# Performance work log

Measured on AMD Instinct MI355X. Metric: run time of the kernel, lower is better.

## Reference

```python
import jax, jax.numpy as jnp
import numpy as np

NH = 12
D = 768
HD = D // NH
F = 3072
EPS = 1e-6
SCALE = 1.0 / np.sqrt(HD).astype(np.float32)


def _ln(x, g, b):
    m = x.mean(-1, keepdims=True)
    v = ((x - m) ** 2).mean(-1, keepdims=True)
    return (x - m) / jnp.sqrt(v + EPS) * g + b


def _heads(t):
    B, S, _ = t.shape
    return t.reshape(B, S, NH, HD).transpose(0, 2, 1, 3)  # [B,H,S,hd]


def _attn(q, k, v):
    # q,k,v: [B,H,S,hd]; dropout rate is 0 so omitted
    s = jnp.einsum('bhqd,bhkd->bhqk', q, k) * SCALE
    p = jax.nn.softmax(s, axis=-1)
    c = jnp.einsum('bhqk,bhkd->bhqd', p, v)
    B, H, S, _ = c.shape
    return c.transpose(0, 2, 1, 3).reshape(B, S, D)


def _mlp(x, W1, b1, W2, b2):
    h = jax.nn.gelu(x @ W1 + b1)  # dropout rate 0.1 -> identity (eval)
    return h @ W2 + b2


def setup_inputs() -> dict:
    key = jax.random.key(0)
    ks = jax.random.split(key, 16)
    B, S = 4, 1024
    rnd = lambda k, sh: (jax.random.normal(k, sh, jnp.float32) * 0.02)
    inp = {
        'x': jax.random.normal(ks[0], (B, S, D), jnp.float32),
        'y': jax.random.normal(ks[1], (B, S, D), jnp.float32),
        'ln1x_g': jnp.ones((D,)), 'ln1x_b': jnp.zeros((D,)),
        'ln1y_g': jnp.ones((D,)), 'ln1y_b': jnp.zeros((D,)),
        'Wq': rnd(ks[2], (D, D)), 'bq': jnp.zeros((D,)),
        'Wk': rnd(ks[3], (D, D)), 'bk': jnp.zeros((D,)),
        'Wv': rnd(ks[4], (D, D)), 'bv': jnp.zeros((D,)),
        'Wo': rnd(ks[5], (D, D)), 'bo': jnp.zeros((D,)),
        'Wqd': rnd(ks[6], (D, D)), 'bqd': jnp.zeros((D,)),
        'Wkd': rnd(ks[7], (D, D)), 'bkd': jnp.zeros((D,)),
        'Wvd': rnd(ks[8], (D, D)), 'bvd': jnp.zeros((D,)),
        'Wod': rnd(ks[9], (D, D)), 'bod': jnp.zeros((D,)),
        'w11': jnp.full((1,), 0.5), 'w12': jnp.full((1,), 0.5),
        'w21': jnp.full((1,), 0.5), 'w22': jnp.full((1,), 0.5),
        'ln2x_g': jnp.ones((D,)), 'ln2x_b': jnp.zeros((D,)),
        'ln2y_g': jnp.ones((D,)), 'ln2y_b': jnp.zeros((D,)),
        'W1': rnd(ks[10], (D, F)), 'b1': jnp.zeros((F,)),
        'W2': rnd(ks[11], (F, D)), 'b2': jnp.zeros((D,)),
        'W1d': rnd(ks[12], (D, F)), 'b1d': jnp.zeros((F,)),
        'W2d': rnd(ks[13], (F, D)), 'b2d': jnp.zeros((D,)),
    }
    return inp


def reference(x, y, ln1x_g, ln1x_b, ln1y_g, ln1y_b,
              Wq, bq, Wk, bk, Wv, bv, Wo, bo,
              Wqd, bqd, Wkd, bkd, Wvd, bvd, Wod, bod,
              w11, w12, w21, w22,
              ln2x_g, ln2x_b, ln2y_g, ln2y_b,
              W1, b1, W2, b2, W1d, b1d, W2d, b2d):
    hx, hy = x, y
    xn = _ln(x, ln1x_g, ln1x_b)
    yn = _ln(y, ln1y_g, ln1y_b)
    q = _heads(xn @ Wq + bq); k = _heads(xn @ Wk + bk); v = _heads(xn @ Wv + bv)
    qd = _heads(yn @ Wqd + bqd); kd = _heads(yn @ Wkd + bkd); vd = _heads(yn @ Wvd + bvd)
    a_sx = _attn(q, k, v) @ Wo + bo          # self-x
    a_sy = _attn(qd, kd, vd) @ Wod + bod     # self-y
    a_cx = _attn(q, kd, vd) @ Wo + bo        # cross x-query into y
    a_cy = _attn(qd, k, v) @ Wod + bod       # cross y-query into x
    ax = w11 * a_sx + w12 * a_cx
    ay = w21 * a_sy + w22 * a_cy
    x = ax + hx
    y = ay + hy
    hx, hy = x, y
    x = _mlp(_ln(x, ln2x_g, ln2x_b), W1, b1, W2, b2) + hx
    y = _mlp(_ln(y, ln2y_g, ln2y_b), W1d, b1d, W2d, b2d) + hy
    return (x, y)
```

## Files before the change

### kernel.cpp

```cpp
#include <hip/hip_runtime.h>

typedef unsigned short u16;
typedef unsigned short u16x8 __attribute__((ext_vector_type(8)));
typedef short s16x8 __attribute__((ext_vector_type(8)));
typedef float f32x4 __attribute__((ext_vector_type(4)));

#define EL ((size_t)3145728)
#define DDE ((size_t)589824)
#define DFE ((size_t)2359296)

#if __has_builtin(__builtin_amdgcn_exp2f)
#define EXP2(x) __builtin_amdgcn_exp2f(x)
#else
#define EXP2(x) __expf((x) * 0.6931471805599453f)
#endif

__device__ __forceinline__ float b2f(u16 u) {
    return __builtin_bit_cast(float, (unsigned)u << 16);
}
__device__ __forceinline__ u16 f2bf(float f) {
    unsigned x = __builtin_bit_cast(unsigned, f);
    return (u16)((x + 0x7fffu + ((x >> 16) & 1u)) >> 16);
}
__device__ __forceinline__ float gelu_f(float x) {
    float t = x + 0.044715f * x * x * x;
    return x * __builtin_amdgcn_rcpf(1.0f + EXP2(-2.302207417f * t));
}
__device__ __forceinline__ f32x4 mfma16(s16x8 a, s16x8 b, f32x4 c) {
    return __builtin_amdgcn_mfma_f32_16x16x32_bf16(a, b, c, 0, 0, 0);
}
__device__ __forceinline__ void gld16(const u16* g, u16* l) {
    __builtin_amdgcn_global_load_lds((const __attribute__((address_space(1))) void*)g,
                                     (__attribute__((address_space(3))) void*)l,
                                     16, 0, 0);
}
__device__ __forceinline__ void xcd_map(int NN, int& m, int& n, int& z, int& ks) {
    int p = blockIdx.x, T = gridDim.x;
    int ppx = T >> 3;
    int xcd = p & 7, l = p >> 3;
    int panel = l / NN;
    n = l - panel * NN;
    int gp = xcd * (ppx / NN) + panel;
    m = gp & 31;
    z = (gp >> 5) & 1;
    ks = gp >> 6;
}

__global__ __launch_bounds__(256) void transpose8_k(const float* p0, const float* p1,
                                                    const float* p2, const float* p3,
                                                    const float* p4, const float* p5,
                                                    const float* p6, const float* p7,
                                                    u16* __restrict__ dst0) {
    int z = blockIdx.z;
    const float* in = z == 0 ? p0 : z == 1 ? p1 : z == 2 ? p2 : z == 3 ? p3
                    : z == 4 ? p4 : z == 5 ? p5 : z == 6 ? p6 : p7;
    u16* out = dst0 + (size_t)z * DDE;
    const int K = 768, N = 768;
    __shared__ u16 tile[64][72];
    int k0 = blockIdx.y << 6, n0 = blockIdx.x << 6;
    int tid = threadIdx.x;
    int r = tid >> 2, c = (tid & 3) << 4;
    const float* ip = in + (size_t)(k0 + r) * N + n0 + c;
#pragma unroll
    for (int q = 0; q < 4; ++q) {
        f32x4 v = *(const f32x4*)(ip + 4 * q);
#pragma unroll
        for (int e = 0; e < 4; ++e) tile[r][c + 4 * q + e] = f2bf(v[e]);
    }
    __syncthreads();
    u16x8 o0, o1;
#pragma unroll
    for (int e = 0; e < 8; ++e) { o0[e] = tile[c + e][r]; o1[e] = tile[c + 8 + e][r]; }
    u16* op = out + (size_t)(n0 + r) * K + k0 + c;
    *(u16x8*)op = o0;
    *(u16x8*)(op + 8) = o1;
}

__global__ __launch_bounds__(256) void transpose2_k(const float* pa, const float* pb,
                                                    u16* __restrict__ dst0, size_t dsz,
                                                    int K, int N) {
    int z = blockIdx.z;
    const float* in = z ? pb : pa;
    u16* out = dst0 + (size_t)z * dsz;
    __shared__ u16 tile[64][72];
    int k0 = blockIdx.y << 6, n0 = blockIdx.x << 6;
    int tid = threadIdx.x;
    int r = tid >> 2, c = (tid & 3) << 4;
    const float* ip = in + (size_t)(k0 + r) * N + n0 + c;
#pragma unroll
    for (int q = 0; q < 4; ++q) {
        f32x4 v = *(const f32x4*)(ip + 4 * q);
#pragma unroll
        for (int e = 0; e < 4; ++e) tile[r][c + 4 * q + e] = f2bf(v[e]);
    }
    __syncthreads();
    u16x8 o0, o1;
#pragma unroll
    for (int e = 0; e < 8; ++e) { o0[e] = tile[c + e][r]; o1[e] = tile[c + 8 + e][r]; }
    u16* op = out + (size_t)(n0 + r) * K + k0 + c;
    *(u16x8*)op = o0;
    *(u16x8*)(op + 8) = o1;
}

__global__ __launch_bounds__(256) void vtrans_k(const u16* __restrict__ Vrow,
                                                u16* __restrict__ VT0) {
    int st = blockIdx.x, bh = blockIdx.y, z = blockIdx.z;
    const u16* src = Vrow + (size_t)z * EL + ((size_t)bh << 16) + (size_t)st * 64 * 64;
    u16* dst = VT0 + (size_t)z * 3 * EL + ((size_t)bh << 16) + st * 64;
    __shared__ u16 tile[64][72];
    int tid = threadIdx.x;
    int r = tid >> 2, c = (tid & 3) << 4;
    const u16* ip = src + (size_t)r * 64 + c;
    u16x8 a = *(const u16x8*)ip;
    u16x8 b = *(const u16x8*)(ip + 8);
#pragma unroll
    for (int e = 0; e < 8; ++e) { tile[r][c + e] = a[e]; tile[r][c + 8 + e] = b[e]; }
    __syncthreads();
    u16x8 o0, o1;
#pragma unroll
    for (int e = 0; e < 8; ++e) { o0[e] = tile[c + e][r]; o1[e] = tile[c + 8 + e][r]; }
    u16* op = dst + (size_t)r * 1024 + c;
    *(u16x8*)op = o0;
    *(u16x8*)(op + 8) = o1;
}

__global__ __launch_bounds__(256) void ln_k(const float* __restrict__ inX,
                                            const float* __restrict__ inY,
                                            const float* gX, const float* bX,
                                            const float* gY, const float* bY,
                                            u16* __restrict__ out0) {
    int z = blockIdx.y;
    const float* in = z ? inY : inX;
    const float* g = z ? gY : gX;
    const float* be = z ? bY : bX;
    u16* out = out0 + (size_t)z * EL;
    int row = blockIdx.x, tid = threadIdx.x;
    const float* p = in + (size_t)row * 768;
    float v0 = p[tid], v1 = p[tid + 256], v2 = p[tid + 512];
    float s = v0 + v1 + v2;
    float q = v0 * v0 + v1 * v1 + v2 * v2;
#pragma unroll
    for (int m = 1; m < 64; m <<= 1) { s += __shfl_xor(s, m); q += __shfl_xor(q, m); }
    __shared__ float red[8];
    int w = tid >> 6, lane = tid & 63;
    if (lane == 0) { red[w] = s; red[4 + w] = q; }
    __syncthreads();
    s = red[0] + red[1] + red[2] + red[3];
    q = red[4] + red[5] + red[6] + red[7];
    float mean = s * (1.0f / 768.0f);
    float var = q * (1.0f / 768.0f) - mean * mean;
    float rstd = rsqrtf(var + 1e-6f);
    u16* o = out + (size_t)row * 768;
    o[tid]       = f2bf((v0 - mean) * rstd * g[tid]       + be[tid]);
    o[tid + 256] = f2bf((v1 - mean) * rstd * g[tid + 256] + be[tid + 256]);
    o[tid + 512] = f2bf((v2 - mean) * rstd * g[tid + 512] + be[tid + 512]);
}

__global__ __launch_bounds__(256) void lnb_k(const u16* __restrict__ inX,
                                             const u16* __restrict__ inY,
                                             const float* gX, const float* bX,
                                             const float* gY, const float* bY,
                                             u16* __restrict__ out0) {
    int z = blockIdx.y;
    const u16* in = z ? inY : inX;
    const float* g = z ? gY : gX;
    const float* be = z ? bY : bX;
    u16* out = out0 + (size_t)z * EL;
    int row = blockIdx.x, tid = threadIdx.x;
    const u16* p = in + (size_t)row * 768;
    float v0 = b2f(p[tid]), v1 = b2f(p[tid + 256]), v2 = b2f(p[tid + 512]);
    float s = v0 + v1 + v2;
    float q = v0 * v0 + v1 * v1 + v2 * v2;
#pragma unroll
    for (int m = 1; m < 64; m <<= 1) { s += __shfl_xor(s, m); q += __shfl_xor(q, m); }
    __shared__ float red[8];
    int w = tid >> 6, lane = tid & 63;
    if (lane == 0) { red[w] = s; red[4 + w] = q; }
    __syncthreads();
    s = red[0] + red[1] + red[2] + red[3];
    q = red[4] + red[5] + red[6] + red[7];
    float mean = s * (1.0f / 768.0f);
    float var = q * (1.0f / 768.0f) - mean * mean;
    float rstd = rsqrtf(var + 1e-6f);
    u16* o = out + (size_t)row * 768;
    o[tid]       = f2bf((v0 - mean) * rstd * g[tid]       + be[tid]);
    o[tid + 256] = f2bf((v1 - mean) * rstd * g[tid + 256] + be[tid + 256]);
    o[tid + 512] = f2bf((v2 - mean) * rstd * g[tid + 512] + be[tid + 512]);
}

__global__ __launch_bounds__(256) void blend_k(u16* __restrict__ a0,
                                               const u16* __restrict__ b0,
                                               const float* w11, const float* w12,
                                               const float* w21, const float* w22,
                                               int n8) {
    int z = blockIdx.z;
    u16* a = a0 + (size_t)z * EL;
    const u16* b = b0 + (size_t)z * EL;
    float wa = z ? *w21 : *w11, wb = z ? *w22 : *w12;
    for (int i = blockIdx.x * blockDim.x + threadIdx.x; i < n8;
         i += gridDim.x * blockDim.x) {
        u16x8 va = ((const u16x8*)a)[i];
        u16x8 vb = ((const u16x8*)b)[i];
        u16x8 r;
#pragma unroll
        for (int e = 0; e < 8; ++e) r[e] = f2bf(wa * b2f(va[e]) + wb * b2f(vb[e]));
        ((u16x8*)a)[i] = r;
    }
}

__global__ __launch_bounds__(256) void combine_k(const float* __restrict__ parts,
                                                 int KS,
                                                 const u16* __restrict__ x1b,
                                                 const float* __restrict__ b2X,
                                                 const float* __restrict__ b2Y,
                                                 float* __restrict__ out, int n4tot) {
    int i = blockIdx.x * 256 + threadIdx.x;
    if (i >= n4tot) return;
    size_t e = (size_t)i * 4;
    f32x4 s = ((const f32x4*)parts)[i];
    for (int k = 1; k < KS; ++k)
        s += ((const f32x4*)(parts + (size_t)k * 2 * EL))[i];
    const float* bb = (e < EL) ? b2X : b2Y;
    int n = (int)(e % 768);
    ushort4 xv = ((const ushort4*)x1b)[i];
    f32x4 r;
    r[0] = s[0] + bb[n]     + b2f(xv.x);
    r[1] = s[1] + bb[n + 1] + b2f(xv.y);
    r[2] = s[2] + bb[n + 2] + b2f(xv.z);
    r[3] = s[3] + bb[n + 3] + b2f(xv.w);
    ((f32x4*)out)[i] = r;
}

#define EPI_GELU 3
#define EPI_WO 4
#define EPI_MLP2 5
#define EPI_PART 6

template <int EPI>
__global__ __launch_bounds__(256) void gemm_k(
    const u16* __restrict__ A0, size_t Asz,
    const u16* __restrict__ B0, size_t Bsz,
    const float* __restrict__ bias0, const float* __restrict__ bias1,
    const void* __restrict__ r0, const void* __restrict__ r1,
    const float* s1a, const float* s1b, const float* s2a, const float* s2b,
    void* __restrict__ C0, size_t Csz,
    int M, int N, int K, int NN, int KS) {
    int m_, n_, z, ks;
    xcd_map(NN, m_, n_, z, ks);
    const int Kloc = K / KS;
    const u16* A = A0 + z * Asz;
    const u16* BT = B0 + z * Bsz;
    const float* bias = z ? bias1 : bias0;
    const float* residf = (const float*)(z ? r1 : r0);
    const u16* residb = (const u16*)(z ? r1 : r0);
    u16* Cb = (u16*)C0 + z * Csz;
    float* Cf = (float*)C0 + ((size_t)ks * 2 + z) * Csz;
    __shared__ u16 lA[2][4096];
    __shared__ u16 lB[2][4096];
    int tid = threadIdx.x;
    int bm0 = m_ << 7, bn0 = n_ << 7;
    int lane = tid & 63, wid = tid >> 6;
    int fr = lane & 15, g = lane >> 4;
    int wm = wid >> 1, wn = wid & 1;
    const u16* srcA0 = A + (size_t)(bm0 + (tid & 127)) * K + ks * Kloc + ((tid >> 7) << 3);
    const u16* srcA1 = srcA0 + 16;
    const u16* srcB0 = BT + (size_t)(bn0 + (tid & 127)) * K + ks * Kloc + ((tid >> 7) << 3);
    const u16* srcB1 = srcB0 + 16;
    auto STAGE = [&](int buf, int k0) {
        gld16(srcA0 + k0, &lA[buf][0] + tid * 8);
        gld16(srcA1 + k0, &lA[buf][0] + 2048 + tid * 8);
        gld16(srcB0 + k0, &lB[buf][0] + tid * 8);
        gld16(srcB1 + k0, &lB[buf][0] + 2048 + tid * 8);
    };
    f32x4 acc[4][4] = {};
    STAGE(0, 0);
    __syncthreads();
    int cur = 0;
    for (int k0 = 0; k0 < Kloc; k0 += 32) {
        if (k0 + 32 < Kloc) STAGE(cur ^ 1, k0 + 32);
        s16x8 af[4], bf[4];
#pragma unroll
        for (int i = 0; i < 4; ++i)
            af[i] = *(const s16x8*)&lA[cur][(g * 128 + wm * 64 + i * 16 + fr) * 8];
#pragma unroll
        for (int j = 0; j < 4; ++j)
            bf[j] = *(const s16x8*)&lB[cur][(g * 128 + wn * 64 + j * 16 + fr) * 8];
#pragma unroll
        for (int i = 0; i < 4; ++i)
#pragma unroll
            for (int j = 0; j < 4; ++j)
                acc[i][j] = mfma16(af[i], bf[j], acc[i][j]);
        __syncthreads();
        cur ^= 1;
    }
    float bscale = 1.0f;
    if (EPI == EPI_WO) bscale = z ? (s2a[0] + s2b[0]) : (s1a[0] + s1b[0]);
#pragma unroll
    for (int j = 0; j < 4; ++j) {
        int n = bn0 + wn * 64 + j * 16 + fr;
        float bv = 0.0f;
        if (EPI != EPI_PART) bv = bias[n] * bscale;
#pragma unroll
        for (int i = 0; i < 4; ++i) {
#pragma unroll
            for (int r = 0; r < 4; ++r) {
                int m = bm0 + wm * 64 + i * 16 + (g << 2) + r;
                size_t idx = (size_t)m * N + n;
                float v = acc[i][j][r] + bv;
                if (EPI == EPI_GELU) {
                    Cb[idx] = f2bf(gelu_f(v));
                } else if (EPI == EPI_WO) {
                    Cb[idx] = f2bf(v + residf[idx]);
                } else if (EPI == EPI_MLP2) {
                    Cf[idx] = v + b2f(residb[idx]);
                } else {
                    Cf[idx] = v;
                }
            }
        }
    }
}

__global__ __launch_bounds__(256) void gemm_qkv_k(const u16* __restrict__ A0,
                                                  const u16* __restrict__ B0,
                                                  const float* bq, const float* bk,
                                                  const float* bv, const float* bqd,
                                                  const float* bkd, const float* bvd,
                                                  u16* __restrict__ Qd,
                                                  u16* __restrict__ Kd,
                                                  u16* __restrict__ Vd) {
    const int K = 768;
    int m_, n_, z, ks_;
    xcd_map(18, m_, n_, z, ks_);
    const u16* A = A0 + z * EL;
    const u16* BT = B0 + z * 3 * DDE;
    __shared__ u16 lA[2][4096];
    __shared__ u16 lB[2][4096];
    int tid = threadIdx.x;
    int bm0 = m_ << 7, bn0 = n_ << 7;
    int lane = tid & 63, wid = tid >> 6, wm = wid >> 1, wn = wid & 1;
    int fr = lane & 15, g = lane >> 4;
    const u16* srcA0 = A + (size_t)(bm0 + (tid & 127)) * K + ((tid >> 7) << 3);
    const u16* srcA1 = srcA0 + 16;
    const u16* srcB0 = BT + (size_t)(bn0 + (tid & 127)) * K + ((tid >> 7) << 3);
    const u16* srcB1 = srcB0 + 16;
    auto STAGE = [&](int buf, int k0) {
        gld16(srcA0 + k0, &lA[buf][0] + tid * 8);
        gld16(srcA1 + k0, &lA[buf][0] + 2048 + tid * 8);
        gld16(srcB0 + k0, &lB[buf][0] + tid * 8);
        gld16(srcB1 + k0, &lB[buf][0] + 2048 + tid * 8);
    };
    f32x4 acc[4][4] = {};
    STAGE(0, 0);
    __syncthreads();
    int cur = 0;
    for (int k0 = 0; k0 < K; k0 += 32) {
        if (k0 + 32 < K) STAGE(cur ^ 1, k0 + 32);
        s16x8 af[4], bf[4];
#pragma unroll
        for (int i = 0; i < 4; ++i)
            af[i] = *(const s16x8*)&lA[cur][(g * 128 + wm * 64 + i * 16 + fr) * 8];
#pragma unroll
        for (int j = 0; j < 4; ++j)
            bf[j] = *(const s16x8*)&lB[cur][(g * 128 + wn * 64 + j * 16 + fr) * 8];
#pragma unroll
        for (int i = 0; i < 4; ++i)
#pragma unroll
            for (int j = 0; j < 4; ++j)
                acc[i][j] = mfma16(af[i], bf[j], acc[i][j]);
        __syncthreads();
        cur ^= 1;
    }
    int seg = bn0 / 768;
    const float* bp = seg == 0 ? (z ? bqd : bq) : seg == 1 ? (z ? bkd : bk) : (z ? bvd : bv);
    u16* out;
    size_t zoff;
    if (seg == 0)      { out = Qd; zoff = (size_t)z * 3 * EL; }
    else if (seg == 1) { out = Kd; zoff = (size_t)z * 3 * EL; }
    else               { out = Vd; zoff = (size_t)z * EL; }
    int nbase = bn0 - seg * 768;
    const float qs = (seg == 0) ? 0.180336880f : 1.0f;
#pragma unroll
    for (int j = 0; j < 4; ++j) {
        int nn = nbase + wn * 64 + j * 16 + fr;
        float bvl = bp[nn];
        int hh = nn >> 6, hd = nn & 63;
#pragma unroll
        for (int i = 0; i < 4; ++i) {
#pragma unroll
            for (int r = 0; r < 4; ++r) {
                int m = bm0 + wm * 64 + i * 16 + (g << 2) + r;
                int bb = m >> 10, ss = m & 1023;
                size_t o = zoff + (((size_t)(bb * 12 + hh)) << 16) + ((size_t)ss << 6) + hd;
                out[o] = f2bf((acc[i][j][r] + bvl) * qs);
            }
        }
    }
}

__global__ __launch_bounds__(256) void attn_k(const u16* __restrict__ Qx,
                                              const u16* __restrict__ Kx,
                                              const u16* __restrict__ VTx,
                                              const u16* __restrict__ Qy,
                                              const u16* __restrict__ Ky,
                                              const u16* __restrict__ VTy,
                                              u16* __restrict__ csx,
                                              u16* __restrict__ ccx,
                                              u16* __restrict__ csy,
                                              u16* __restrict__ ccy) {
    int p = blockIdx.x;
    int lg = (p & 7) * 192 + (p >> 3);
    int sg = lg >> 4, wi = lg & 15;
    int qt = wi & 7, sub = wi >> 3;
    int pairi = sg / 48, bh = sg % 48;
    int cfg = pairi == 0 ? (sub ? 3 : 0) : (sub ? 2 : 1);
    const u16 *Qp, *Kp, *Vp;
    u16* Op;
    if (cfg == 0)      { Qp = Qx; Kp = Kx; Vp = VTx; Op = csx; }
    else if (cfg == 1) { Qp = Qy; Kp = Ky; Vp = VTy; Op = csy; }
    else if (cfg == 2) { Qp = Qx; Kp = Ky; Vp = VTy; Op = ccx; }
    else               { Qp = Qy; Kp = Kx; Vp = VTx; Op = ccy; }
    const u16* Qh = Qp + ((size_t)bh << 16);
    const u16* Kh = Kp + ((size_t)bh << 16);
    const u16* Vh = Vp + ((size_t)bh << 16);
    int b = bh / 12, h = bh % 12;
    int tid = threadIdx.x, lane = tid & 63, w = tid >> 6;
    int q0 = qt * 128 + w * 32;
    int fr = lane & 15, ko = (lane >> 4) << 3, g = lane >> 4;
    bool glo = lane < 32;
    int srcA = fr + ((lane & 16) << 1);
    int srcB = srcA + 16;

    __shared__ u16 kls[4096];
    __shared__ u16 vls[4096];

    s16x8 qf[2][2];
#pragma unroll
    for (int s = 0; s < 2; ++s) {
        const u16* qp = Qh + (size_t)(q0 + s * 16 + fr) * 64 + ko;
        qf[s][0] = *(const s16x8*)qp;
        qf[s][1] = *(const s16x8*)(qp + 32);
    }

    f32x4 acc[2][4] = {};
    float lsum[2] = {0.f, 0.f};
    f32x4 zz = {0.f, 0.f, 0.f, 0.f};

    int krow = tid >> 3, kpc = tid & 7;
    int kgc = kpc ^ (krow & 7);
    int vdr = tid >> 2, vpv = tid & 3;
    int cK0 = ((fr << 3) + (g ^ (fr & 7))) << 3;
    int cK1 = ((fr << 3) + ((g + 4) ^ (fr & 7))) << 3;
    int cK2 = (((fr + 16) << 3) + (g ^ (fr & 7))) << 3;
    int cK3 = (((fr + 16) << 3) + ((g + 4) ^ (fr & 7))) << 3;

    auto HALF = [&](int base) {
        s16x8 Kf0 = *(const s16x8*)&kls[base + cK0];
        s16x8 Kf1 = *(const s16x8*)&kls[base + cK1];
        s16x8 Kf2 = *(const s16x8*)&kls[base + cK2];
        s16x8 Kf3 = *(const s16x8*)&kls[base + cK3];
        s16x8 Vf[4];
#pragma unroll
        for (int t4 = 0; t4 < 4; ++t4)
            Vf[t4] = *(const s16x8*)&vls[base + ((t4 * 16 + fr) << 5) + (g << 3)];
        s16x8 pa[2];
#pragma unroll
        for (int s = 0; s < 2; ++s) {
            __builtin_amdgcn_s_setprio(1);
            f32x4 t0 = mfma16(Kf0, qf[s][0], zz);
            t0 = mfma16(Kf1, qf[s][1], t0);
            f32x4 t1 = mfma16(Kf2, qf[s][0], zz);
            t1 = mfma16(Kf3, qf[s][1], t1);
            __builtin_amdgcn_s_setprio(0);
            float p00 = EXP2(t0[0]), p01 = EXP2(t0[1]);
            float p02 = EXP2(t0[2]), p03 = EXP2(t0[3]);
            float p10 = EXP2(t1[0]), p11 = EXP2(t1[1]);
            float p12 = EXP2(t1[2]), p13 = EXP2(t1[3]);
            lsum[s] += (p00 + p01 + p02 + p03) + (p10 + p11 + p12 + p13);
            unsigned w0, w1, w2, w3;
            asm("v_cvt_pk_bf16_f32 %0, %1, %2" : "=v"(w0) : "v"(p00), "v"(p01));
            asm("v_cvt_pk_bf16_f32 %0, %1, %2" : "=v"(w1) : "v"(p02), "v"(p03));
            asm("v_cvt_pk_bf16_f32 %0, %1, %2" : "=v"(w2) : "v"(p10), "v"(p11));
            asm("v_cvt_pk_bf16_f32 %0, %1, %2" : "=v"(w3) : "v"(p12), "v"(p13));
            int e0 = __shfl((int)w0, srcA), e1 = __shfl((int)w1, srcA);
            int e2 = __shfl((int)w0, srcB), e3 = __shfl((int)w1, srcB);
            int f0 = __shfl((int)w2, srcA), f1 = __shfl((int)w3, srcA);
            int f2 = __shfl((int)w2, srcB), f3 = __shfl((int)w3, srcB);
            int4 wd;
            wd.x = glo ? e0 : f0;
            wd.y = glo ? e1 : f1;
            wd.z = glo ? e2 : f2;
            wd.w = glo ? e3 : f3;
            pa[s] = __builtin_bit_cast(s16x8, wd);
        }
        __builtin_amdgcn_s_setprio(1);
#pragma unroll
        for (int t4 = 0; t4 < 4; ++t4) {
            acc[0][t4] = mfma16(pa[0], Vf[t4], acc[0][t4]);
            acc[1][t4] = mfma16(pa[1], Vf[t4], acc[1][t4]);
        }
        __builtin_amdgcn_s_setprio(0);
    };

    for (int kb = 0; kb < 1024; kb += 64) {
        gld16(Kh + (size_t)(kb + krow) * 64 + kgc * 8, &kls[tid * 8]);
        gld16(Kh + (size_t)(kb + 32 + krow) * 64 + kgc * 8, &kls[2048 + tid * 8]);
        gld16(Vh + (size_t)vdr * 1024 + kb + vpv * 8, &vls[tid * 8]);
        gld16(Vh + (size_t)vdr * 1024 + kb + 32 + vpv * 8, &vls[2048 + tid * 8]);
        __syncthreads();
        HALF(0);
        HALF(2048);
        __syncthreads();
    }

    float invv[2][4];
#pragma unroll
    for (int s = 0; s < 2; ++s) {
        float l = lsum[s];
        l += __shfl_xor(l, 16);
        l += __shfl_xor(l, 32);
        float inv = 1.0f / l;
#pragma unroll
        for (int r = 0; r < 4; ++r)
            invv[s][r] = __shfl(inv, ((lane >> 4) << 2) + r);
    }
#pragma unroll
    for (int s = 0; s < 2; ++s) {
        u16* ob = Op + (size_t)(b * 1024 + q0 + s * 16 + ((lane >> 4) << 2)) * 768 + h * 64 + fr;
#pragma unroll
        for (int t4 = 0; t4 < 4; ++t4)
#pragma unroll
            for (int r = 0; r < 4; ++r)
                ob[(size_t)r * 768 + t4 * 16] = f2bf(acc[s][t4][r] * invv[s][r]);
    }
}

extern "C" void kernel_launch(void* const* d_in, const int* in_sizes, int n_in,
                              void* d_out, int out_size, void* d_ws, size_t ws_size,
                              hipStream_t stream) {
    (void)in_sizes; (void)n_in; (void)out_size;
    const float* X    = (const float*)d_in[0];
    const float* Y    = (const float*)d_in[1];
    const float* l1xg = (const float*)d_in[2];
    const float* l1xb = (const float*)d_in[3];
    const float* l1yg = (const float*)d_in[4];
    const float* l1yb = (const float*)d_in[5];
    const float* Wq   = (const float*)d_in[6];
    const float* bq   = (const float*)d_in[7];
    const float* Wk   = (const float*)d_in[8];
    const float* bk   = (const float*)d_in[9];
    const float* Wv   = (const float*)d_in[10];
    const float* bv   = (const float*)d_in[11];
    const float* Wo   = (const float*)d_in[12];
    const float* bo   = (const float*)d_in[13];
    const float* Wqd  = (const float*)d_in[14];
    const float* bqd  = (const float*)d_in[15];
    const float* Wkd  = (const float*)d_in[16];
    const float* bkd  = (const float*)d_in[17];
    const float* Wvd  = (const float*)d_in[18];
    const float* bvd  = (const float*)d_in[19];
    const float* Wod  = (const float*)d_in[20];
    const float* bod  = (const float*)d_in[21];
    const float* w11  = (const float*)d_in[22];
    const float* w12  = (const float*)d_in[23];
    const float* w21  = (const float*)d_in[24];
    const float* w22  = (const float*)d_in[25];
    const float* l2xg = (const float*)d_in[26];
    const float* l2xb = (const float*)d_in[27];
    const float* l2yg = (const float*)d_in[28];
    const float* l2yb = (const float*)d_in[29];
    const float* W1   = (const float*)d_in[30];
    const float* b1   = (const float*)d_in[31];
    const float* W2   = (const float*)d_in[32];
    const float* b2   = (const float*)d_in[33];
    const float* W1d  = (const float*)d_in[34];
    const float* b1d  = (const float*)d_in[35];
    const float* W2d  = (const float*)d_in[36];
    const float* b2d  = (const float*)d_in[37];

    u16* ws = (u16*)d_ws;
    u16* qkvT = ws;
    u16* WoT  = qkvT + 6 * DDE;
    u16* W1T  = WoT + 2 * DDE;
    u16* W2T  = W1T + 2 * DFE;
    u16* xn   = W2T + 2 * DFE;
    u16* Qx   = xn + 2 * EL;
    u16* cs   = Qx + 6 * EL;
    u16* x1   = cs + 4 * EL;
    u16* Kx = Qx + EL;
    u16* VTx = Qx + 2 * EL;
    u16* h = Qx;
    u16* y1 = x1 + EL;
    u16* wsEnd = x1 + 2 * EL;
    u16* Vrow = cs;

    float* out_x = (float*)d_out;

    float* parts = (float*)wsEnd;
    size_t baseBytes = (size_t)(wsEnd - ws) * 2;
    size_t partBytes = 2 * EL * sizeof(float);
    int KS = 1;
    if (ws_size >= baseBytes + 4 * partBytes) KS = 4;
    else if (ws_size >= baseBytes + 2 * partBytes) KS = 2;

    dim3 tb(256);
    transpose8_k<<<dim3(12, 12, 8), tb, 0, stream>>>(Wq, Wk, Wv, Wqd, Wkd, Wvd, Wo, Wod, qkvT);
    transpose2_k<<<dim3(48, 12, 2), tb, 0, stream>>>(W1, W1d, W1T, DFE, 768, 3072);
    transpose2_k<<<dim3(12, 48, 2), tb, 0, stream>>>(W2, W2d, W2T, DFE, 3072, 768);
    ln_k<<<dim3(4096, 2), tb, 0, stream>>>(X, Y, l1xg, l1xb, l1yg, l1yb, xn);
    gemm_qkv_k<<<1152, tb, 0, stream>>>(xn, qkvT, bq, bk, bv, bqd, bkd, bvd,
                                        Qx, Kx, Vrow);
    vtrans_k<<<dim3(16, 48, 2), tb, 0, stream>>>(Vrow, VTx);
    attn_k<<<4 * 48 * 8, tb, 0, stream>>>(Qx, Kx, VTx, Qx + 3 * EL, Qx + 4 * EL, Qx + 5 * EL,
                                          cs, cs + 2 * EL, cs + EL, cs + 3 * EL);
    int n8 = (int)(EL / 8);
    blend_k<<<dim3(1536, 1, 2), tb, 0, stream>>>(cs, cs + 2 * EL, w11, w12, w21, w22, n8);
    gemm_k<EPI_WO><<<384, tb, 0, stream>>>(
        cs, EL, WoT, DDE, bo, bod, X, Y, w11, w12, w21, w22, x1, EL,
        4096, 768, 768, 6, 1);
    lnb_k<<<dim3(4096, 2), tb, 0, stream>>>(x1, y1, l2xg, l2xb, l2yg, l2yb, xn);
    gemm_k<EPI_GELU><<<1536, tb, 0, stream>>>(
        xn, EL, W1T, DFE, b1, b1d, nullptr, nullptr, nullptr, nullptr, nullptr, nullptr,
        h, 4 * EL, 4096, 3072, 768, 24, 1);
    if (KS > 1) {
        gemm_k<EPI_PART><<<384 * KS, tb, 0, stream>>>(
            h, 4 * EL, W2T, DFE, nullptr, nullptr, nullptr, nullptr,
            nullptr, nullptr, nullptr, nullptr,
            parts, EL, 4096, 768, 3072, 6, KS);
        int n4 = (int)(2 * EL / 4);
        combine_k<<<(n4 + 255) / 256, tb, 0, stream>>>(parts, KS, x1, b2, b2d,
                                                       out_x, n4);
    } else {
        gemm_k<EPI_MLP2><<<384, tb, 0, stream>>>(
            h, 4 * EL, W2T, DFE, b2, b2d, x1, y1,
            nullptr, nullptr, nullptr, nullptr,
            out_x, EL, 4096, 768, 3072, 6, 1);
    }
}
```

Baseline: 427.0 us.

## Share K/V tiles between self and cross attention in 512-thread blocks

The attention kernel now runs 512-thread blocks where two wavegroups share one K/V head. One wavegroup computes self attention and the other computes cross attention with the other stream's queries. Each K/V tile is loaded into LDS once per block and used by both query sets, which halves global K/V traffic and the block count. The cost is larger blocks with higher register and LDS pressure per CU, which may lower occupancy or scheduling flexibility.

```diff
diff --git a/kernel.cpp b/kernel.cpp
--- a/kernel.cpp
+++ b/kernel.cpp
@@ -398,7 +398,7 @@
     }
 }
 
-__global__ __launch_bounds__(256) void attn_k(const u16* __restrict__ Qx,
+__global__ __launch_bounds__(512) void attn_k(const u16* __restrict__ Qx,
                                               const u16* __restrict__ Kx,
                                               const u16* __restrict__ VTx,
                                               const u16* __restrict__ Qy,
@@ -409,22 +409,22 @@
                                               u16* __restrict__ csy,
                                               u16* __restrict__ ccy) {
     int p = blockIdx.x;
-    int lg = (p & 7) * 192 + (p >> 3);
-    int sg = lg >> 4, wi = lg & 15;
-    int qt = wi & 7, sub = wi >> 3;
+    int lg = (p & 7) * 96 + (p >> 3);
+    int sg = lg >> 3, qt = lg & 7;
     int pairi = sg / 48, bh = sg % 48;
-    int cfg = pairi == 0 ? (sub ? 3 : 0) : (sub ? 2 : 1);
-    const u16 *Qp, *Kp, *Vp;
+    int tid = threadIdx.x, lane = tid & 63, wid = tid >> 6;
+    int wg = wid >> 2, w = wid & 3;
+    int cfg = pairi == 0 ? (wg ? 3 : 0) : (wg ? 2 : 1);
+    const u16* Kh = (pairi ? Ky : Kx) + ((size_t)bh << 16);
+    const u16* Vh = (pairi ? VTy : VTx) + ((size_t)bh << 16);
+    const u16* Qp;
     u16* Op;
-    if (cfg == 0)      { Qp = Qx; Kp = Kx; Vp = VTx; Op = csx; }
-    else if (cfg == 1) { Qp = Qy; Kp = Ky; Vp = VTy; Op = csy; }
-    else if (cfg == 2) { Qp = Qx; Kp = Ky; Vp = VTy; Op = ccx; }
-    else               { Qp = Qy; Kp = Kx; Vp = VTx; Op = ccy; }
+    if (cfg == 0)      { Qp = Qx; Op = csx; }
+    else if (cfg == 1) { Qp = Qy; Op = csy; }
+    else if (cfg == 2) { Qp = Qx; Op = ccx; }
+    else               { Qp = Qy; Op = ccy; }
     const u16* Qh = Qp + ((size_t)bh << 16);
-    const u16* Kh = Kp + ((size_t)bh << 16);
-    const u16* Vh = Vp + ((size_t)bh << 16);
     int b = bh / 12, h = bh % 12;
-    int tid = threadIdx.x, lane = tid & 63, w = tid >> 6;
     int q0 = qt * 128 + w * 32;
     int fr = lane & 15, ko = (lane >> 4) << 3, g = lane >> 4;
     bool glo = lane < 32;
@@ -446,9 +446,11 @@
     float lsum[2] = {0.f, 0.f};
     f32x4 zz = {0.f, 0.f, 0.f, 0.f};
 
-    int krow = tid >> 3, kpc = tid & 7;
+    int half = tid >> 8, tt = tid & 255;
+    int krow = tt >> 3, kpc = tt & 7;
     int kgc = kpc ^ (krow & 7);
-    int vdr = tid >> 2, vpv = tid & 3;
+    int vdr = tt >> 2, vpv = tt & 3;
+    int lbase = half * 2048 + tt * 8;
     int cK0 = ((fr << 3) + (g ^ (fr & 7))) << 3;
     int cK1 = ((fr << 3) + ((g + 4) ^ (fr & 7))) << 3;
     int cK2 = (((fr + 16) << 3) + (g ^ (fr & 7))) << 3;
@@ -503,10 +505,8 @@
     };
 
     for (int kb = 0; kb < 1024; kb += 64) {
-        gld16(Kh + (size_t)(kb + krow) * 64 + kgc * 8, &kls[tid * 8]);
-        gld16(Kh + (size_t)(kb + 32 + krow) * 64 + kgc * 8, &kls[2048 + tid * 8]);
-        gld16(Vh + (size_t)vdr * 1024 + kb + vpv * 8, &vls[tid * 8]);
-        gld16(Vh + (size_t)vdr * 1024 + kb + 32 + vpv * 8, &vls[2048 + tid * 8]);
+        gld16(Kh + (size_t)(kb + half * 32 + krow) * 64 + kgc * 8, &kls[lbase]);
+        gld16(Vh + (size_t)vdr * 1024 + kb + half * 32 + vpv * 8, &vls[lbase]);
         __syncthreads();
         HALF(0);
         HALF(2048);
@@ -611,7 +611,7 @@
     gemm_qkv_k<<<1152, tb, 0, stream>>>(xn, qkvT, bq, bk, bv, bqd, bkd, bvd,
                                         Qx, Kx, Vrow);
     vtrans_k<<<dim3(16, 48, 2), tb, 0, stream>>>(Vrow, VTx);
-    attn_k<<<4 * 48 * 8, tb, 0, stream>>>(Qx, Kx, VTx, Qx + 3 * EL, Qx + 4 * EL, Qx + 5 * EL,
+    attn_k<<<768, dim3(512), 0, stream>>>(Qx, Kx, VTx, Qx + 3 * EL, Qx + 4 * EL, Qx + 5 * EL,
                                           cs, cs + 2 * EL, cs + EL, cs + 3 * EL);
     int n8 = (int)(EL / 8);
     blend_k<<<dim3(1536, 1, 2), tb, 0, stream>>>(cs, cs + 2 * EL, w11, w12, w21, w22, n8);
```

Result: slower. 437.3 us (+2.4%).
